# Kernel tuning notes

Hardware: AMD Instinct MI355X
Metric: run time of the kernel (lower is better)

Reference implementation:

```python
import jax, jax.numpy as jnp
import numpy as np

B, T, C = 2, 2048, 2048
N_HEAD, N_KV_HEAD = 16, 4
HEAD_DIM = C // N_HEAD  # 128
HALF = HEAD_DIM // 2    # 64


def _rms_norm(x):
    # F.rms_norm with no weight: x / sqrt(mean(x^2) + eps), eps = dtype eps
    eps = jnp.finfo(x.dtype).eps
    return x * jax.lax.rsqrt(jnp.mean(x * x, axis=-1, keepdims=True) + eps)


def _rope_apply(x, cos, sin):
    # x: [B, H, T, Hs]; cos/sin: [1, 1, T, Hs/2]
    x1, x2 = x[..., :HALF], x[..., HALF:]
    return jnp.concatenate([x1 * cos - x2 * sin, x1 * sin + x2 * cos], axis=-1)


def setup_inputs() -> dict:
    key = jax.random.key(0)
    ks = jax.random.split(key, 8)
    x = jax.random.normal(ks[0], (B, T, C), dtype=jnp.float32)
    # real RoPE tables (base 10000), shape [1,1,T,HALF]
    inv_freq = 1.0 / (10000.0 ** (np.arange(0, HALF, dtype=np.float32) / HALF))
    t = np.arange(T, dtype=np.float32)
    ang = np.einsum('t,f->tf', t, inv_freq)
    cos = jnp.asarray(np.cos(ang))[None, None]
    sin = jnp.asarray(np.sin(ang))[None, None]
    s = 0.02
    Wq = jax.random.normal(ks[1], (C, N_HEAD * HEAD_DIM), dtype=jnp.float32) * s
    Wk = jax.random.normal(ks[2], (C, N_KV_HEAD * HEAD_DIM), dtype=jnp.float32) * s
    Wv = jax.random.normal(ks[3], (C, N_KV_HEAD * HEAD_DIM), dtype=jnp.float32) * s
    Wo = jax.random.normal(ks[4], (C, C), dtype=jnp.float32) * s
    bo = jnp.zeros((C,), dtype=jnp.float32)
    return {"x": x, "cos": cos, "sin": sin, "Wq": Wq, "Wk": Wk, "Wv": Wv, "Wo": Wo, "bo": bo}


def reference(x, cos, sin, Wq, Wk, Wv, Wo, bo):
    Bq, Tq, Cq = x.shape
    G = N_HEAD // N_KV_HEAD
    # QKV projections (GQA, no bias)
    q = (x @ Wq).reshape(Bq, Tq, N_HEAD, HEAD_DIM)
    k = (x @ Wk).reshape(Bq, Tq, N_KV_HEAD, HEAD_DIM)
    v = (x @ Wv).reshape(Bq, Tq, N_KV_HEAD, HEAD_DIM)
    # QK RMSNorm (over head_dim), then to [B, H, T, Hs]
    q = jnp.transpose(_rms_norm(q), (0, 2, 1, 3))
    k = jnp.transpose(_rms_norm(k), (0, 2, 1, 3))
    v = jnp.transpose(v, (0, 2, 1, 3))
    # RoPE
    q = _rope_apply(q, cos[:, :, :Tq, :], sin[:, :, :Tq, :])
    k = _rope_apply(k, cos[:, :, :Tq, :], sin[:, :, :Tq, :])
    # GQA: repeat kv heads across groups
    k = jnp.repeat(k, G, axis=1)  # [B, H, T, Hs]
    v = jnp.repeat(v, G, axis=1)
    # Causal SDPA
    scale = 1.0 / jnp.sqrt(jnp.asarray(HEAD_DIM, dtype=x.dtype))
    scores = jnp.einsum('bhqd,bhkd->bhqk', q, k) * scale
    causal = jnp.tril(jnp.ones((Tq, Tq), dtype=bool))
    scores = jnp.where(causal, scores, jnp.asarray(-jnp.inf, dtype=scores.dtype))
    attn = jax.nn.softmax(scores, axis=-1)
    y = jnp.einsum('bhqk,bhkd->bhqd', attn, v)
    y = jnp.transpose(y, (0, 2, 1, 3)).reshape(Bq, Tq, Cq)
    return y @ Wo + bo
```

## Files before the change

### kernel.cpp

```cpp
#include <hip/hip_runtime.h>
#include <hip/hip_bf16.h>
#include <math.h>

#define BB 2
#define TT 2048
#define CC 2048
#define NH 16
#define NKV 4
#define HD 128
#define HALF 64
#define MTOT (BB*TT)
#define NQKV (CC + 2*NKV*HD)

typedef unsigned short u16;
typedef __attribute__((ext_vector_type(8))) short bf16x8;
typedef __attribute__((ext_vector_type(4))) float f32x4;

__device__ __forceinline__ u16 f2bf(float f) {
  unsigned u = __float_as_uint(f);
  unsigned r = (u + 0x7FFFu + ((u >> 16) & 1u)) >> 16;
  return (u16)r;
}
__device__ __forceinline__ u16 f2bf_hw(float f) {
  __hip_bfloat16 h = __float2bfloat16(f);
  return *reinterpret_cast<const u16*>(&h);
}
__device__ __forceinline__ float bf2f(u16 v) {
  return __uint_as_float(((unsigned)v) << 16);
}

__device__ __forceinline__ void gl_lds16(const void* g, void* l) {
  __builtin_amdgcn_global_load_lds(
      (const __attribute__((address_space(1))) unsigned int*)g,
      (__attribute__((address_space(3))) unsigned int*)l, 16, 0, 0);
}

__device__ __forceinline__ int xcd_swz(int bid, int nwg) {
  return (bid & 7) * (nwg >> 3) + (bid >> 3);
}

__global__ __launch_bounds__(256) void prep(
    const float* __restrict__ x, const float* __restrict__ Wq,
    const float* __restrict__ Wk, const float* __restrict__ Wv,
    const float* __restrict__ Wo, u16* __restrict__ xb,
    u16* __restrict__ Wt, u16* __restrict__ Wot) {
  const int z = blockIdx.z;
  const int tx = threadIdx.x, ty = threadIdx.y;
  if (z == 4) {
    const int tid = ty * 32 + tx;
    const int i = (blockIdx.y * 64 + blockIdx.x) * 256 + tid;
    const float4* s4 = (const float4*)x;
    float4 a = s4[(size_t)i * 2], b = s4[(size_t)i * 2 + 1];
    bf16x8 o;
    o[0] = (short)f2bf(a.x); o[1] = (short)f2bf(a.y);
    o[2] = (short)f2bf(a.z); o[3] = (short)f2bf(a.w);
    o[4] = (short)f2bf(b.x); o[5] = (short)f2bf(b.y);
    o[6] = (short)f2bf(b.z); o[7] = (short)f2bf(b.w);
    ((bf16x8*)xb)[i] = o;
    return;
  }
  const float* W; u16* dst; int N; int row_off;
  if (z == 0)      { W = Wq; dst = Wt;  N = 2048; row_off = 0; }
  else if (z == 1) { W = Wk; dst = Wt;  N = 512;  row_off = 2048; }
  else if (z == 2) { W = Wv; dst = Wt;  N = 512;  row_off = 2560; }
  else             { W = Wo; dst = Wot; N = 2048; row_off = 0; }
  const int n0 = blockIdx.x * 32, k0 = blockIdx.y * 32;
  if (n0 >= N) return;
  __shared__ float tile[32][33];
#pragma unroll
  for (int i = 0; i < 4; ++i)
    tile[ty + 8 * i][tx] = W[(size_t)(k0 + ty + 8 * i) * N + n0 + tx];
  __syncthreads();
#pragma unroll
  for (int i = 0; i < 4; ++i)
    dst[(size_t)(row_off + n0 + ty + 8 * i) * CC + k0 + tx] =
        f2bf(tile[tx][ty + 8 * i]);
}

__global__ __launch_bounds__(256, 2) void gemm_128(
    const u16* __restrict__ A, const u16* __restrict__ Bt,
    const float* __restrict__ bias, float* __restrict__ C,
    int M, int N, int K, int out_bf16) {
  __shared__ u16 As[16384];
  __shared__ u16 Bs[16384];
  const int tid = threadIdx.x;
  const int w = tid >> 6, lane = tid & 63;
  const int quad = lane >> 4, lo = lane & 15;
  const int wm = w >> 1, wn = w & 1;
  const int nwg = gridDim.x * gridDim.y;
  const int swz = xcd_swz(blockIdx.y * gridDim.x + blockIdx.x, nwg);
  const int bm = (swz / gridDim.x) * 128, bn = (swz % gridDim.x) * 128;
  const int NT = K >> 6;

  const u16* agp[2][2]; const u16* bgp[2][2];
#pragma unroll
  for (int h = 0; h < 2; ++h)
#pragma unroll
    for (int j = 0; j < 2; ++j) {
      const unsigned X = (unsigned)h * 8192u +
                         (unsigned)((w * 2 + j) * 64 + lane) * 16u;
      const int row = (int)(X >> 7);
      const int ce = (int)(((X & 127u) ^ (((X >> 7) & 7u) << 4)) >> 1);
      agp[h][j] = A  + (size_t)(bm + row) * K + ce;
      bgp[h][j] = Bt + (size_t)(bn + row) * K + ce;
    }
  char* const lAs = (char*)As;
  char* const lBs = (char*)Bs;
  const int woff = w * 2048;

#define STGA8(hh, bufp, kt) do { \
    gl_lds16(agp[hh][0] + (size_t)(kt) * 64, lAs + (bufp) * 16384 + (hh) * 8192 + woff); \
    gl_lds16(agp[hh][1] + (size_t)(kt) * 64, lAs + (bufp) * 16384 + (hh) * 8192 + woff + 1024); \
  } while (0)
#define STGB8(hh, bufp, kt) do { \
    gl_lds16(bgp[hh][0] + (size_t)(kt) * 64, lBs + (bufp) * 16384 + (hh) * 8192 + woff); \
    gl_lds16(bgp[hh][1] + (size_t)(kt) * 64, lBs + (bufp) * 16384 + (hh) * 8192 + woff + 1024); \
  } while (0)

  const int sw  = (lo & 7) << 4;
  const int co0 = (quad * 16) ^ sw;
  const int co1 = (64 + quad * 16) ^ sw;
  const int aRB = (wm * 64 + lo) * 128;
  const int bRB = (wn * 64 + lo) * 128;

  f32x4 acc[4][4];
#pragma unroll
  for (int i = 0; i < 4; ++i)
#pragma unroll
    for (int ci = 0; ci < 4; ++ci)
#pragma unroll
      for (int r = 0; r < 4; ++r) acc[i][ci][r] = 0.f;

  STGA8(0, 0, 0); STGA8(1, 0, 0); STGB8(0, 0, 0); STGB8(1, 0, 0);
  STGB8(0, 1, 1); STGB8(1, 1, 1); STGA8(0, 1, 1);
  asm volatile("s_waitcnt vmcnt(6)" ::: "memory");
  __builtin_amdgcn_s_barrier();

  for (int t = 0; t < NT; ++t) {
    const int pa = t & 1;
    const char* Ab = lAs + pa * 16384 + aRB;
    const char* Bb = lBs + pa * 16384 + bRB;
    bf16x8 a[4][2], b[4][2];
#pragma unroll
    for (int i = 0; i < 4; ++i) {
      a[i][0] = *(const bf16x8*)(Ab + i * 2048 + co0);
      a[i][1] = *(const bf16x8*)(Ab + i * 2048 + co1);
    }
#pragma unroll
    for (int ci = 0; ci < 4; ++ci) {
      b[ci][0] = *(const bf16x8*)(Bb + ci * 2048 + co0);
      b[ci][1] = *(const bf16x8*)(Bb + ci * 2048 + co1);
    }
    if (t + 1 < NT) STGA8(1, (t + 1) & 1, t + 1);
    asm volatile("s_waitcnt lgkmcnt(0)");
    __builtin_amdgcn_s_barrier();
    __builtin_amdgcn_s_setprio(1);
#pragma unroll
    for (int i = 0; i < 4; ++i)
#pragma unroll
      for (int ci = 0; ci < 2; ++ci) {
        acc[i][ci] = __builtin_amdgcn_mfma_f32_16x16x32_bf16(a[i][0], b[ci][0], acc[i][ci], 0, 0, 0);
        acc[i][ci] = __builtin_amdgcn_mfma_f32_16x16x32_bf16(a[i][1], b[ci][1], acc[i][ci], 0, 0, 0);
      }
    __builtin_amdgcn_s_setprio(0);
    if (t + 2 < NT) { STGB8(0, pa, t + 2); STGB8(1, pa, t + 2); STGA8(0, pa, t + 2); }
    if (t + 2 < NT)      asm volatile("s_waitcnt vmcnt(6)" ::: "memory");
    else if (t + 1 < NT) asm volatile("s_waitcnt vmcnt(0)" ::: "memory");
    __builtin_amdgcn_s_setprio(1);
#pragma unroll
    for (int i = 0; i < 4; ++i)
#pragma unroll
      for (int ci = 2; ci < 4; ++ci) {
        acc[i][ci] = __builtin_amdgcn_mfma_f32_16x16x32_bf16(a[i][0], b[ci][0], acc[i][ci], 0, 0, 0);
        acc[i][ci] = __builtin_amdgcn_mfma_f32_16x16x32_bf16(a[i][1], b[ci][1], acc[i][ci], 0, 0, 0);
      }
    __builtin_amdgcn_s_setprio(0);
    __builtin_amdgcn_s_barrier();
  }
#undef STGA8
#undef STGB8

  const int rbase = bm + wm * 64;
  const int cbase = bn + wn * 64;
#pragma unroll
  for (int i = 0; i < 4; ++i)
#pragma unroll
    for (int ci = 0; ci < 4; ++ci) {
      const int col = cbase + ci * 16 + lo;
      const float bv = bias ? bias[col] : 0.f;
#pragma unroll
      for (int r = 0; r < 4; ++r) {
        const int row = rbase + i * 16 + quad * 4 + r;
        const float v = acc[i][ci][r] + bv;
        if (out_bf16) ((u16*)C)[(size_t)row * N + col] = f2bf(v);
        else          C[(size_t)row * N + col] = v;
      }
    }
}

__global__ __launch_bounds__(256) void qkv_post(
    const u16* __restrict__ qkv_lin, const float* __restrict__ cosp,
    const float* __restrict__ sinp, u16* __restrict__ q, u16* __restrict__ k,
    u16* __restrict__ vt) {
  __shared__ u16 tile[32][33];
  if (blockIdx.y == 5) {
    const int bx = blockIdx.x;
    if (bx >= 2048) return;
    const int t0 = (bx & 63) * 32, d0 = ((bx >> 6) & 3) * 32;
    const int p = bx >> 8;
    const int b = p >> 2, kv = p & 3;
    const int tx = threadIdx.x & 31, ty = threadIdx.x >> 5;
#pragma unroll
    for (int i = 0; i < 4; ++i)
      tile[ty + 8 * i][tx] =
          qkv_lin[(size_t)(b * TT + t0 + ty + 8 * i) * NQKV + CC + NKV * HD + kv * HD + d0 + tx];
    __syncthreads();
    const int tperm = ((tx >> 2) & 3) * 8 + (tx & 3) + 4 * ((tx >> 4) & 1);
#pragma unroll
    for (int i = 0; i < 4; ++i)
      vt[((size_t)p * HD + d0 + ty + 8 * i) * TT + t0 + tperm] = tile[tx][ty + 8 * i];
    return;
  }
  const int bt = blockIdx.x;
  const int hh = blockIdx.y * 4 + (threadIdx.x >> 6);
  const int lane = threadIdx.x & 63;
  const int lam = lane & 31;
  const int t = bt & (TT - 1), b = bt >> 11;
  const int col = (hh < NH) ? hh * HD : CC + (hh - NH) * HD;
  const u16* src = qkv_lin + (size_t)bt * NQKV + col;
  const unsigned wv = *(const unsigned*)(src + 2 * lane);
  const float e0 = bf2f((u16)(wv & 0xFFFFu)), e1 = bf2f((u16)(wv >> 16));
  float ss = e0 * e0 + e1 * e1;
#pragma unroll
  for (int mm = 1; mm < 64; mm <<= 1) ss += __shfl_xor(ss, mm, 64);
  const float rms = rsqrtf(ss * (1.f / 128.f) + 1.1920929e-7f);
  const unsigned w1 = (unsigned)__shfl((int)wv, lam, 64);
  const unsigned w2 = (unsigned)__shfl((int)wv, lam + 32, 64);
  const float x1a = bf2f((u16)(w1 & 0xFFFFu)), x1b = bf2f((u16)(w1 >> 16));
  const float x2a = bf2f((u16)(w2 & 0xFFFFu)), x2b = bf2f((u16)(w2 >> 16));
  const float2 cs = *(const float2*)(cosp + t * HALF + 2 * lam);
  const float2 sn = *(const float2*)(sinp + t * HALF + 2 * lam);
  float oa, ob;
  if (lane < 32) {
    oa = x1a * rms * cs.x - x2a * rms * sn.x;
    ob = x1b * rms * cs.y - x2b * rms * sn.y;
  } else {
    oa = x1a * rms * sn.x + x2a * rms * cs.x;
    ob = x1b * rms * sn.y + x2b * rms * cs.y;
  }
  const unsigned ow = (unsigned)f2bf(oa) | ((unsigned)f2bf(ob) << 16);
  u16* dst = (hh < NH)
      ? q + (((size_t)(b * NH + hh)) * TT + t) * HD
      : k + (((size_t)(b * NKV + (hh - NH))) * TT + t) * HD;
  *(unsigned*)(dst + 2 * lane) = ow;
}

__device__ __forceinline__ void softmax_pack(
    const f32x4* sacc, float& l_lane, bf16x8* ap, int rowq, int t0,
    bool diag, int quad) {
  const float cc = 0.12751744050808612f;
  float e[4][4];
  if (diag) {
#pragma unroll
    for (int ct = 0; ct < 4; ++ct)
#pragma unroll
      for (int r = 0; r < 4; ++r) {
        float v = __builtin_amdgcn_exp2f(sacc[ct][r] * cc);
        if (t0 + ct * 16 + quad * 4 + r > rowq) v = 0.f;
        l_lane += v; e[ct][r] = v;
      }
  } else {
#pragma unroll
    for (int ct = 0; ct < 4; ++ct)
#pragma unroll
      for (int r = 0; r < 4; ++r) {
        float v = __builtin_amdgcn_exp2f(sacc[ct][r] * cc);
        l_lane += v; e[ct][r] = v;
      }
  }
#pragma unroll
  for (int k2 = 0; k2 < 2; ++k2) {
    bf16x8 ch;
#pragma unroll
    for (int j = 0; j < 8; ++j)
      ch[j] = (short)f2bf_hw(e[k2 * 2 + (j >> 2)][j & 3]);
    ap[k2] = ch;
  }
}

__global__ __launch_bounds__(512, 4) void attn_mfma(
    const u16* __restrict__ Qb, const u16* __restrict__ Kb,
    const u16* __restrict__ Vt, u16* __restrict__ Y) {
  __shared__ u16 Ks[2][8192];
  __shared__ u16 Vs[2][8192];

  const int fid = blockIdx.y * (int)gridDim.x + blockIdx.x;
  const int xcd = fid & 7, slot = fid >> 3;
  const int qt = slot & 15;
  const int bh = xcd * 4 + (slot >> 4);
  const int b = bh >> 4, h = bh & 15, kvh = h >> 2;
  const int tid = threadIdx.x;
  const int wave = tid >> 6, lane = tid & 63;
  const int wg = wave >> 2, wv = wave & 3;
  const int quad = lane >> 4, lo = lane & 15;

  const int rows = (wg == 0) ? qt * 64 : (31 - qt) * 64;
  const u16* Qg = Qb + (size_t)(b * NH + h) * TT * HD;
  const u16* Kg = Kb + (size_t)(b * NKV + kvh) * TT * HD;
  const u16* Vg = Vt + (size_t)(b * NKV + kvh) * HD * TT;

  bf16x8 aq[4];
#pragma unroll
  for (int kc = 0; kc < 4; ++kc)
    aq[kc] = *(const bf16x8*)(Qg + (size_t)(rows + wv * 16 + lo) * HD + kc * 32 + quad * 8);

  const u16* kgp[2]; const u16* vgp[2];
  u16* klp[2][2]; u16* vlp[2][2];
#pragma unroll
  for (int c = 0; c < 2; ++c) {
    const int s = wave * 2 + c;
    const int ct = s >> 2, kq = s & 3;
    kgp[c] = Kg + (size_t)(ct * 16 + lo) * HD + kq * 32 + quad * 8;
    const int dt = s >> 1, k2 = s & 1;
    vgp[c] = Vg + (size_t)(dt * 16 + lo) * TT + k2 * 32 + quad * 8;
    klp[0][c] = &Ks[0][s * 512]; klp[1][c] = &Ks[1][s * 512];
    vlp[0][c] = &Vs[0][s * 512]; vlp[1][c] = &Vs[1][s * 512];
  }

  f32x4 oacc[8];
#pragma unroll
  for (int dt = 0; dt < 8; ++dt)
#pragma unroll
    for (int r = 0; r < 4; ++r) oacc[dt][r] = 0.f;
  float l_lane = 0.f;

  const int ntiles = 32 - qt;
  const int rowq = rows + wv * 16 + lo;

#pragma unroll
  for (int c = 0; c < 2; ++c) {
    gl_lds16(kgp[c], klp[0][c]); kgp[c] += 64 * HD;
    gl_lds16(vgp[c], vlp[0][c]); vgp[c] += 64;
  }

  for (int nt = 0; nt < ntiles; ++nt) {
    const int par = nt & 1;
    __syncthreads();
    if (nt + 1 < ntiles) {
#pragma unroll
      for (int c = 0; c < 2; ++c) {
        gl_lds16(kgp[c], klp[par ^ 1][c]); kgp[c] += 64 * HD;
        gl_lds16(vgp[c], vlp[par ^ 1][c]); vgp[c] += 64;
      }
    }
    const bool act = (wg == 1) || (nt <= qt);
    if (act) {
      const u16* ksb = Ks[par];
      const u16* vsb = Vs[par];
      const int t0 = nt * 64;

      f32x4 sacc[4];
#pragma unroll
      for (int ct = 0; ct < 4; ++ct)
#pragma unroll
        for (int r = 0; r < 4; ++r) sacc[ct][r] = 0.f;
      __builtin_amdgcn_s_setprio(1);
#pragma unroll
      for (int ct = 0; ct < 4; ++ct)
#pragma unroll
        for (int kc = 0; kc < 4; ++kc) {
          bf16x8 bk = *(const bf16x8*)&ksb[(ct * 4 + kc) * 512 + lane * 8];
          sacc[ct] = __builtin_amdgcn_mfma_f32_16x16x32_bf16(bk, aq[kc], sacc[ct], 0, 0, 0);
        }
      __builtin_amdgcn_s_setprio(0);

      bf16x8 ap[2];
      softmax_pack(sacc, l_lane, ap, rowq, t0, t0 + 63 > rows + wv * 16, quad);

      __builtin_amdgcn_s_setprio(1);
#pragma unroll
      for (int dt = 0; dt < 8; ++dt)
#pragma unroll
        for (int k2 = 0; k2 < 2; ++k2) {
          bf16x8 bv = *(const bf16x8*)&vsb[(dt * 2 + k2) * 512 + lane * 8];
          oacc[dt] = __builtin_amdgcn_mfma_f32_16x16x32_bf16(ap[k2], bv, oacc[dt], 0, 0, 0);
        }
      __builtin_amdgcn_s_setprio(0);
    }
  }

  float l = l_lane;
  l += __shfl_xor(l, 16, 64);
  l += __shfl_xor(l, 32, 64);
  l = 1.f / l;
  float linv[4];
#pragma unroll
  for (int r = 0; r < 4; ++r)
    linv[r] = __shfl(l, quad * 4 + r, 64);
  const size_t row0 = (size_t)b * TT + rows + wv * 16 + quad * 4;
#pragma unroll
  for (int dt = 0; dt < 8; ++dt)
#pragma unroll
    for (int r = 0; r < 4; ++r)
      Y[(row0 + r) * CC + h * HD + dt * 16 + lo] = f2bf(oacc[dt][r] * linv[r]);
}

extern "C" void kernel_launch(void* const* d_in, const int* in_sizes, int n_in,
                              void* d_out, int out_size, void* d_ws, size_t ws_size,
                              hipStream_t stream) {
  (void)in_sizes; (void)n_in; (void)out_size; (void)ws_size;
  const float* x    = (const float*)d_in[0];
  const float* cosp = (const float*)d_in[1];
  const float* sinp = (const float*)d_in[2];
  const float* Wq   = (const float*)d_in[3];
  const float* Wk   = (const float*)d_in[4];
  const float* Wv   = (const float*)d_in[5];
  const float* Wo   = (const float*)d_in[6];
  const float* bo   = (const float*)d_in[7];
  float* out = (float*)d_out;
  char* ws = (char*)d_ws;

  const size_t MB = 1024 * 1024;
  u16* xb      = (u16*)(ws);
  u16* Wt      = (u16*)(ws + 16 * MB);
  u16* qkv_lin = (u16*)(ws + 28 * MB);
  u16* Wot     = (u16*)(ws + 52 * MB);
  u16* qb_buf  = (u16*)(ws);
  u16* kb      = (u16*)(ws + 16 * MB);
  u16* vt      = (u16*)(ws + 20 * MB);
  u16* y       = (u16*)(ws + 28 * MB);

  prep<<<dim3(64, 64, 5), dim3(32, 8), 0, stream>>>(x, Wq, Wk, Wv, Wo, xb, Wt, Wot);

  gemm_128<<<dim3(NQKV / 128, MTOT / 128), 256, 0, stream>>>(
      xb, Wt, nullptr, (float*)qkv_lin, MTOT, NQKV, CC, 1);

  qkv_post<<<dim3(MTOT, 6), 256, 0, stream>>>(qkv_lin, cosp, sinp, qb_buf, kb, vt);

  attn_mfma<<<dim3(16, BB * NH), 512, 0, stream>>>(qb_buf, kb, vt, y);

  gemm_128<<<dim3(CC / 128, MTOT / 128), 256, 0, stream>>>(
      y, Wot, bo, out, MTOT, CC, CC, 0);
}
```

Measured before the change: 306.5 us.

## Fuse QK RMSNorm, RoPE and V transpose into QKV GEMM epilogue

The QKV GEMM changes its warp layout so each wave owns 32 rows by all 128 columns, which equals one full head per tile. That lets the epilogue compute the per-row RMS norm with a 16-lane shuffle and apply RoPE directly, writing q/k in head-major layout. V tiles are transposed through shared memory and written as permuted vt. This removes the separate qkv_post kernel and the round trip of the bf16 qkv_lin intermediate through memory. In exchange, the GEMM reads more B fragments per wave (8 versus 4) and the output GEMM has a different register and LDS-read balance.

```diff
diff --git a/kernel.cpp b/kernel.cpp
--- a/kernel.cpp
+++ b/kernel.cpp
@@ -80,13 +80,13 @@
 __global__ __launch_bounds__(256, 2) void gemm_128(
     const u16* __restrict__ A, const u16* __restrict__ Bt,
     const float* __restrict__ bias, float* __restrict__ C,
-    int M, int N, int K, int out_bf16) {
-  __shared__ u16 As[16384];
-  __shared__ u16 Bs[16384];
+    int M, int N, int K, int out_bf16, int fuse,
+    const float* __restrict__ cosp, const float* __restrict__ sinp,
+    u16* __restrict__ qout, u16* __restrict__ kout, u16* __restrict__ vtout) {
+  __shared__ u16 SH[32768];
   const int tid = threadIdx.x;
   const int w = tid >> 6, lane = tid & 63;
   const int quad = lane >> 4, lo = lane & 15;
-  const int wm = w >> 1, wn = w & 1;
   const int nwg = gridDim.x * gridDim.y;
   const int swz = xcd_swz(blockIdx.y * gridDim.x + blockIdx.x, nwg);
   const int bm = (swz / gridDim.x) * 128, bn = (swz % gridDim.x) * 128;
@@ -104,8 +104,8 @@
       agp[h][j] = A  + (size_t)(bm + row) * K + ce;
       bgp[h][j] = Bt + (size_t)(bn + row) * K + ce;
     }
-  char* const lAs = (char*)As;
-  char* const lBs = (char*)Bs;
+  char* const lAs = (char*)SH;
+  char* const lBs = (char*)(SH + 16384);
   const int woff = w * 2048;
 
 #define STGA8(hh, bufp, kt) do { \
@@ -120,14 +120,14 @@
   const int sw  = (lo & 7) << 4;
   const int co0 = (quad * 16) ^ sw;
   const int co1 = (64 + quad * 16) ^ sw;
-  const int aRB = (wm * 64 + lo) * 128;
-  const int bRB = (wn * 64 + lo) * 128;
-
-  f32x4 acc[4][4];
-#pragma unroll
-  for (int i = 0; i < 4; ++i)
-#pragma unroll
-    for (int ci = 0; ci < 4; ++ci)
+  const int aRB = (w * 32 + lo) * 128;
+  const int bRB = lo * 128;
+
+  f32x4 acc[2][8];
+#pragma unroll
+  for (int i = 0; i < 2; ++i)
+#pragma unroll
+    for (int ci = 0; ci < 8; ++ci)
 #pragma unroll
       for (int r = 0; r < 4; ++r) acc[i][ci][r] = 0.f;
 
@@ -140,14 +140,14 @@
     const int pa = t & 1;
     const char* Ab = lAs + pa * 16384 + aRB;
     const char* Bb = lBs + pa * 16384 + bRB;
-    bf16x8 a[4][2], b[4][2];
-#pragma unroll
-    for (int i = 0; i < 4; ++i) {
+    bf16x8 a[2][2], b[8][2];
+#pragma unroll
+    for (int i = 0; i < 2; ++i) {
       a[i][0] = *(const bf16x8*)(Ab + i * 2048 + co0);
       a[i][1] = *(const bf16x8*)(Ab + i * 2048 + co1);
     }
 #pragma unroll
-    for (int ci = 0; ci < 4; ++ci) {
+    for (int ci = 0; ci < 8; ++ci) {
       b[ci][0] = *(const bf16x8*)(Bb + ci * 2048 + co0);
       b[ci][1] = *(const bf16x8*)(Bb + ci * 2048 + co1);
     }
@@ -156,9 +156,9 @@
     __builtin_amdgcn_s_barrier();
     __builtin_amdgcn_s_setprio(1);
 #pragma unroll
-    for (int i = 0; i < 4; ++i)
-#pragma unroll
-      for (int ci = 0; ci < 2; ++ci) {
+    for (int i = 0; i < 2; ++i)
+#pragma unroll
+      for (int ci = 0; ci < 4; ++ci) {
         acc[i][ci] = __builtin_amdgcn_mfma_f32_16x16x32_bf16(a[i][0], b[ci][0], acc[i][ci], 0, 0, 0);
         acc[i][ci] = __builtin_amdgcn_mfma_f32_16x16x32_bf16(a[i][1], b[ci][1], acc[i][ci], 0, 0, 0);
       }
@@ -168,9 +168,9 @@
     else if (t + 1 < NT) asm volatile("s_waitcnt vmcnt(0)" ::: "memory");
     __builtin_amdgcn_s_setprio(1);
 #pragma unroll
-    for (int i = 0; i < 4; ++i)
-#pragma unroll
-      for (int ci = 2; ci < 4; ++ci) {
+    for (int i = 0; i < 2; ++i)
+#pragma unroll
+      for (int ci = 4; ci < 8; ++ci) {
         acc[i][ci] = __builtin_amdgcn_mfma_f32_16x16x32_bf16(a[i][0], b[ci][0], acc[i][ci], 0, 0, 0);
         acc[i][ci] = __builtin_amdgcn_mfma_f32_16x16x32_bf16(a[i][1], b[ci][1], acc[i][ci], 0, 0, 0);
       }
@@ -180,79 +180,86 @@
 #undef STGA8
 #undef STGB8
 
-  const int rbase = bm + wm * 64;
-  const int cbase = bn + wn * 64;
-#pragma unroll
-  for (int i = 0; i < 4; ++i)
-#pragma unroll
-    for (int ci = 0; ci < 4; ++ci) {
-      const int col = cbase + ci * 16 + lo;
-      const float bv = bias ? bias[col] : 0.f;
+  if (!fuse) {
+    const int rbase = bm + w * 32;
+#pragma unroll
+    for (int i = 0; i < 2; ++i)
+#pragma unroll
+      for (int ci = 0; ci < 8; ++ci) {
+        const int col = bn + ci * 16 + lo;
+        const float bv = bias ? bias[col] : 0.f;
+#pragma unroll
+        for (int r = 0; r < 4; ++r) {
+          const int row = rbase + i * 16 + quad * 4 + r;
+          const float v = acc[i][ci][r] + bv;
+          if (out_bf16) ((u16*)C)[(size_t)row * N + col] = f2bf(v);
+          else          C[(size_t)row * N + col] = v;
+        }
+      }
+    return;
+  }
+
+  const int htile = bn >> 7;
+  if (htile < 20) {
+#pragma unroll
+    for (int i = 0; i < 2; ++i) {
+      float ss[4];
 #pragma unroll
       for (int r = 0; r < 4; ++r) {
-        const int row = rbase + i * 16 + quad * 4 + r;
-        const float v = acc[i][ci][r] + bv;
-        if (out_bf16) ((u16*)C)[(size_t)row * N + col] = f2bf(v);
-        else          C[(size_t)row * N + col] = v;
-      }
-    }
-}
-
-__global__ __launch_bounds__(256) void qkv_post(
-    const u16* __restrict__ qkv_lin, const float* __restrict__ cosp,
-    const float* __restrict__ sinp, u16* __restrict__ q, u16* __restrict__ k,
-    u16* __restrict__ vt) {
-  __shared__ u16 tile[32][33];
-  if (blockIdx.y == 5) {
-    const int bx = blockIdx.x;
-    if (bx >= 2048) return;
-    const int t0 = (bx & 63) * 32, d0 = ((bx >> 6) & 3) * 32;
-    const int p = bx >> 8;
-    const int b = p >> 2, kv = p & 3;
-    const int tx = threadIdx.x & 31, ty = threadIdx.x >> 5;
-#pragma unroll
-    for (int i = 0; i < 4; ++i)
-      tile[ty + 8 * i][tx] =
-          qkv_lin[(size_t)(b * TT + t0 + ty + 8 * i) * NQKV + CC + NKV * HD + kv * HD + d0 + tx];
+        float s2 = 0.f;
+#pragma unroll
+        for (int ci = 0; ci < 8; ++ci) s2 += acc[i][ci][r] * acc[i][ci][r];
+        ss[r] = s2;
+      }
+#pragma unroll
+      for (int mm = 1; mm < 16; mm <<= 1)
+#pragma unroll
+        for (int r = 0; r < 4; ++r) ss[r] += __shfl_xor(ss[r], mm, 64);
+#pragma unroll
+      for (int r = 0; r < 4; ++r) {
+        const float rmsv = rsqrtf(ss[r] * (1.f / 128.f) + 1.1920929e-7f);
+        const int row = bm + w * 32 + i * 16 + quad * 4 + r;
+        const int bb = row >> 11, tt = row & (TT - 1);
+        u16* dst = (htile < NH)
+            ? qout + (((size_t)(bb * NH + htile)) * TT + tt) * HD
+            : kout + (((size_t)(bb * NKV + (htile - NH))) * TT + tt) * HD;
+#pragma unroll
+        for (int ci = 0; ci < 4; ++ci) {
+          const int d = ci * 16 + lo;
+          const float c = cosp[tt * HALF + d], s = sinp[tt * HALF + d];
+          const float x1 = acc[i][ci][r] * rmsv;
+          const float x2 = acc[i][ci + 4][r] * rmsv;
+          dst[d]      = f2bf(x1 * c - x2 * s);
+          dst[d + 64] = f2bf(x1 * s + x2 * c);
+        }
+      }
+    }
+  } else {
+    const int kv = htile - 20;
     __syncthreads();
-    const int tperm = ((tx >> 2) & 3) * 8 + (tx & 3) + 4 * ((tx >> 4) & 1);
-#pragma unroll
-    for (int i = 0; i < 4; ++i)
-      vt[((size_t)p * HD + d0 + ty + 8 * i) * TT + t0 + tperm] = tile[tx][ty + 8 * i];
-    return;
-  }
-  const int bt = blockIdx.x;
-  const int hh = blockIdx.y * 4 + (threadIdx.x >> 6);
-  const int lane = threadIdx.x & 63;
-  const int lam = lane & 31;
-  const int t = bt & (TT - 1), b = bt >> 11;
-  const int col = (hh < NH) ? hh * HD : CC + (hh - NH) * HD;
-  const u16* src = qkv_lin + (size_t)bt * NQKV + col;
-  const unsigned wv = *(const unsigned*)(src + 2 * lane);
-  const float e0 = bf2f((u16)(wv & 0xFFFFu)), e1 = bf2f((u16)(wv >> 16));
-  float ss = e0 * e0 + e1 * e1;
-#pragma unroll
-  for (int mm = 1; mm < 64; mm <<= 1) ss += __shfl_xor(ss, mm, 64);
-  const float rms = rsqrtf(ss * (1.f / 128.f) + 1.1920929e-7f);
-  const unsigned w1 = (unsigned)__shfl((int)wv, lam, 64);
-  const unsigned w2 = (unsigned)__shfl((int)wv, lam + 32, 64);
-  const float x1a = bf2f((u16)(w1 & 0xFFFFu)), x1b = bf2f((u16)(w1 >> 16));
-  const float x2a = bf2f((u16)(w2 & 0xFFFFu)), x2b = bf2f((u16)(w2 >> 16));
-  const float2 cs = *(const float2*)(cosp + t * HALF + 2 * lam);
-  const float2 sn = *(const float2*)(sinp + t * HALF + 2 * lam);
-  float oa, ob;
-  if (lane < 32) {
-    oa = x1a * rms * cs.x - x2a * rms * sn.x;
-    ob = x1b * rms * cs.y - x2b * rms * sn.y;
-  } else {
-    oa = x1a * rms * sn.x + x2a * rms * cs.x;
-    ob = x1b * rms * sn.y + x2b * rms * cs.y;
-  }
-  const unsigned ow = (unsigned)f2bf(oa) | ((unsigned)f2bf(ob) << 16);
-  u16* dst = (hh < NH)
-      ? q + (((size_t)(b * NH + hh)) * TT + t) * HD
-      : k + (((size_t)(b * NKV + (hh - NH))) * TT + t) * HD;
-  *(unsigned*)(dst + 2 * lane) = ow;
+#pragma unroll
+    for (int i = 0; i < 2; ++i)
+#pragma unroll
+      for (int ci = 0; ci < 8; ++ci)
+#pragma unroll
+        for (int r = 0; r < 4; ++r)
+          SH[(ci * 16 + lo) * 136 + w * 32 + i * 16 + quad * 4 + r] =
+              f2bf(acc[i][ci][r]);
+    __syncthreads();
+    const int p = (bm >> 11) * NKV + kv;
+    const int t0g = bm & (TT - 1);
+    const int tl = lane & 31;
+    const int tp = ((tl >> 2) & 3) * 8 + (tl & 3) + 4 * ((tl >> 4) & 1);
+#pragma unroll
+    for (int dd = 0; dd < 32; ++dd) {
+      const int d = w * 32 + dd;
+#pragma unroll
+      for (int tc = 0; tc < 2; ++tc) {
+        const u16 v = SH[d * 136 + tc * 64 + lane];
+        vtout[((size_t)p * HD + d) * TT + t0g + tc * 64 + (lane & 32) + tp] = v;
+      }
+    }
+  }
 }
 
 __device__ __forceinline__ void softmax_pack(
@@ -421,24 +428,23 @@
   char* ws = (char*)d_ws;
 
   const size_t MB = 1024 * 1024;
-  u16* xb      = (u16*)(ws);
-  u16* Wt      = (u16*)(ws + 16 * MB);
-  u16* qkv_lin = (u16*)(ws + 28 * MB);
-  u16* Wot     = (u16*)(ws + 52 * MB);
-  u16* qb_buf  = (u16*)(ws);
-  u16* kb      = (u16*)(ws + 16 * MB);
-  u16* vt      = (u16*)(ws + 20 * MB);
-  u16* y       = (u16*)(ws + 28 * MB);
+  u16* xb     = (u16*)(ws);
+  u16* Wt     = (u16*)(ws + 16 * MB);
+  u16* kb     = (u16*)(ws + 28 * MB);
+  u16* vt     = (u16*)(ws + 32 * MB);
+  u16* qb_buf = (u16*)(ws + 36 * MB);
+  u16* Wot    = (u16*)(ws + 52 * MB);
+  u16* y      = (u16*)(ws);
 
   prep<<<dim3(64, 64, 5), dim3(32, 8), 0, stream>>>(x, Wq, Wk, Wv, Wo, xb, Wt, Wot);
 
   gemm_128<<<dim3(NQKV / 128, MTOT / 128), 256, 0, stream>>>(
-      xb, Wt, nullptr, (float*)qkv_lin, MTOT, NQKV, CC, 1);
-
-  qkv_post<<<dim3(MTOT, 6), 256, 0, stream>>>(qkv_lin, cosp, sinp, qb_buf, kb, vt);
+      xb, Wt, nullptr, nullptr, MTOT, NQKV, CC, 1, 1,
+      cosp, sinp, qb_buf, kb, vt);
 
   attn_mfma<<<dim3(16, BB * NH), 512, 0, stream>>>(qb_buf, kb, vt, y);
 
   gemm_128<<<dim3(CC / 128, MTOT / 128), 256, 0, stream>>>(
-      y, Wot, bo, out, MTOT, CC, CC, 0);
-}
+      y, Wot, bo, out, MTOT, CC, CC, 0, 0,
+      nullptr, nullptr, nullptr, nullptr, nullptr);
+}
```

Result: faster. 290.0 us (-5.4%).
